# Optimization experiments

Measured on AMD Instinct MI355X. Metric: run time of the kernel, lower is better.

## Reference

```python
import jax, jax.numpy as jnp
import numpy as np
import math

DIM = 768
MAX_STEP = 4
B, S = 32, 2048
LN_EPS = 1e-5
NORM_EPS = 1e-12


def _ln_relu(x, g, b):
    mu = jnp.mean(x, axis=-1, keepdims=True)
    var = jnp.mean((x - mu) ** 2, axis=-1, keepdims=True)
    return jax.nn.relu((x - mu) * jax.lax.rsqrt(var + LN_EPS) * g + b)


def _l2norm(v):  # torch F.normalize along dim=1
    n = jnp.sqrt(jnp.sum(v * v, axis=1, keepdims=True))
    return v / jnp.maximum(n, NORM_EPS)


def setup_inputs() -> dict:
    key = jax.random.key(0)
    ks = jax.random.split(key, 16)
    d = DIM
    inp = {
        "step": 0,
        "context": jax.random.normal(ks[0], (B, S, d), jnp.float32),
        "question": jax.random.normal(ks[1], (B, d), jnp.float32),
        "control": jax.random.normal(ks[2], (B, 2 * d), jnp.float32),
        "qm1": jax.random.randint(ks[3], (B, S), 0, 2).astype(jnp.float32),
        "qm2": jax.random.randint(ks[4], (B, S), 0, 2).astype(jnp.float32),
        "qm_l1": jax.random.randint(ks[5], (B,), 0, S).astype(jnp.int32),
        "qm_l2": jax.random.randint(ks[6], (B,), 0, S).astype(jnp.int32),
        # parameters (xavier-ish scale)
        "W_pos": jax.random.normal(ks[7], (MAX_STEP, d, d), jnp.float32) * (1.0 / math.sqrt(d)),
        "b_pos": jnp.zeros((MAX_STEP, d), jnp.float32),
        "ln1_g": jnp.ones((d,), jnp.float32), "ln1_b": jnp.zeros((d,), jnp.float32),
        "W_cq": jax.random.normal(ks[8], (3 * d, d), jnp.float32) * (1.0 / math.sqrt(3 * d)),
        "b_cq": jnp.zeros((d,), jnp.float32),
        "ln2_g": jnp.ones((d,), jnp.float32), "ln2_b": jnp.zeros((d,), jnp.float32),
        "W_attn": jax.random.normal(ks[9], (d, 1), jnp.float32) * (1.0 / math.sqrt(d)),
        "b_attn": jnp.zeros((1,), jnp.float32),
        "W_fuse": jax.random.normal(ks[10], (2 * d, d), jnp.float32) * (1.0 / math.sqrt(2 * d)),
        "b_fuse": jnp.zeros((d,), jnp.float32),
        "ln3_g": jnp.ones((d,), jnp.float32), "ln3_b": jnp.zeros((d,), jnp.float32),
        "ln4_g": jnp.ones((d,), jnp.float32), "ln4_b": jnp.zeros((d,), jnp.float32),
    }
    return inp


def reference(step, context, question, control, qm1, qm2, qm_l1, qm_l2,
              W_pos, b_pos, ln1_g, ln1_b, W_cq, b_cq, ln2_g, ln2_b,
              W_attn, b_attn, W_fuse, b_fuse, ln3_g, ln3_b, ln4_g, ln4_b):
    d = context.shape[-1]
    scale = 1.0 / math.sqrt(d)
    qm = qm1 + qm2  # [B,S]

    pa = _ln_relu(question @ W_pos[step] + b_pos[step], ln1_g, ln1_b)  # [B,d]
    cq = _ln_relu(jnp.concatenate([control, pa], axis=1) @ W_cq + b_cq, ln2_g, ln2_b)
    cqu = cq[:, None, :]  # [B,1,d]

    def scores(x, mask):  # x:[B,S,d], mask:[B,S]
        w = (x @ W_attn + b_attn) * scale  # [B,S,1] (dropout is identity in eval)
        w = jnp.where(mask[:, :, None] == 0, -1e9, w)
        return jax.nn.softmax(w, axis=1)

    attn = scores(cqu * context, qm)                     # [B,S,1]
    masked_ctx1 = context * qm1[:, :, None]
    masked_ctx2 = context * qm2[:, :, None]
    attn1 = scores(cqu * masked_ctx1, qm1)
    attn2 = scores(cqu * masked_ctx2, qm2)

    mc1 = _l2norm(jnp.sum(attn1 * masked_ctx1, axis=1))  # [B,d]
    mc2 = _l2norm(jnp.sum(attn2 * masked_ctx2, axis=1))
    ncf = _l2norm(jnp.sum(attn * context, axis=1))

    ctrl1 = _ln_relu(jnp.concatenate([mc1, ncf], axis=1) @ W_fuse + b_fuse, ln3_g, ln3_b)
    ctrl2 = _ln_relu(jnp.concatenate([mc2, ncf], axis=1) @ W_fuse + b_fuse, ln4_g, ln4_b)

    next_control = jnp.concatenate([ctrl1, ctrl2], axis=1)  # [B,2d]
    attentions = jnp.concatenate([attn[:, None], attn1[:, None], attn2[:, None]], axis=1)  # [B,3,S,1]
    return next_control, attentions
```

## Files before the change

### kernel.cpp

```cpp
#include <hip/hip_runtime.h>
#include <hip/hip_bf16.h>
#include <math.h>

#define DIM   768
#define BATCH 32
#define SEQ   2048
#define SCALE 0.036084391824351615f

__device__ __forceinline__ float wave_sum(float v) {
#pragma unroll
    for (int o = 32; o > 0; o >>= 1) v += __shfl_xor(v, o, 64);
    return v;
}

__device__ __forceinline__ void fma4(float4& a, float s, const float4& c) {
    a.x += s * c.x; a.y += s * c.y; a.z += s * c.z; a.w += s * c.w;
}

__global__ __launch_bounds__(256) void gemm_partial(
        const float* __restrict__ A0, int lda0,
        const float* __restrict__ A1, int lda1, int ksplit,
        const float* __restrict__ W,
        float* __restrict__ part, int Mtot,
        const int* __restrict__ step_ptr, int wstride) {
    const float* Wp = W + (step_ptr ? (long)step_ptr[0] * wstride : 0);
    const int jt = blockIdx.x * 64;
    const int r0 = blockIdx.y * 32;
    const int kc = blockIdx.z;
    __shared__ float As[32][33];
    __shared__ float Ws[32][64];
    const int t = threadIdx.x;
    const int j = t & 63;
    const int bg = t >> 6;
    float acc[8];
#pragma unroll
    for (int i = 0; i < 8; i++) acc[i] = 0.f;

    for (int k0 = kc * 64; k0 < kc * 64 + 64; k0 += 32) {
        {
            int r  = t >> 3;
            int kk = (t & 7) * 4;
            int ka = k0 + kk;
            float4 av;
            if (ka < ksplit)
                av = *(const float4*)(A0 + (long)(r0 + r) * lda0 + ka);
            else
                av = *(const float4*)(A1 + (long)(r0 + r) * lda1 + (ka - ksplit));
            As[r][kk] = av.x; As[r][kk + 1] = av.y; As[r][kk + 2] = av.z; As[r][kk + 3] = av.w;
        }
#pragma unroll
        for (int i = 0; i < 2; i++) {
            int idx = t + i * 256;
            int row = idx >> 4, col4 = idx & 15;
            float4 wv = *(const float4*)(Wp + (long)(k0 + row) * DIM + jt + col4 * 4);
            *(float4*)&Ws[row][col4 * 4] = wv;
        }
        __syncthreads();
#pragma unroll 8
        for (int kk = 0; kk < 32; kk++) {
            float wv = Ws[kk][j];
#pragma unroll
            for (int i = 0; i < 8; i++) acc[i] += As[bg * 8 + i][kk] * wv;
        }
        __syncthreads();
    }
#pragma unroll
    for (int i = 0; i < 8; i++)
        part[((long)(kc * Mtot + r0 + bg * 8 + i)) * DIM + jt + j] = acc[i];
}

__global__ __launch_bounds__(256) void reduce_ln(
        const float* __restrict__ part, int KC, int Mtot,
        const float* __restrict__ bias,
        const int* __restrict__ step_ptr, int bstride,
        const float* __restrict__ g, const float* __restrict__ b,
        const float* __restrict__ wattn,
        float* __restrict__ out) {
    const int row = blockIdx.x;
    const int t = threadIdx.x;
    const float* bp = bias + (step_ptr ? (long)step_ptr[0] * bstride : 0);
    __shared__ float r1[4], r2[4];
    float x[3];
    float s = 0.f, ss = 0.f;
#pragma unroll
    for (int i = 0; i < 3; i++) {
        int jj = t + i * 256;
        float v = bp[jj];
#pragma unroll 4
        for (int kc = 0; kc < KC; kc++)
            v += part[((long)(kc * Mtot + row)) * DIM + jj];
        x[i] = v; s += v; ss += v * v;
    }
    float wsv = wave_sum(s), wss = wave_sum(ss);
    int lane = t & 63, wid = t >> 6;
    if (lane == 0) { r1[wid] = wsv; r2[wid] = wss; }
    __syncthreads();
    s  = r1[0] + r1[1] + r1[2] + r1[3];
    ss = r2[0] + r2[1] + r2[2] + r2[3];
    float mu = s * (1.f / DIM);
    float var = ss * (1.f / DIM) - mu * mu;
    float rs = rsqrtf(var + 1e-5f);
#pragma unroll
    for (int i = 0; i < 3; i++) {
        int jj = t + i * 256;
        float y = (x[i] - mu) * rs * g[jj] + b[jj];
        y = y > 0.f ? y : 0.f;
        if (wattn) y *= wattn[jj];
        out[(long)row * DIM + jj] = y;
    }
}

__global__ __launch_bounds__(256) void reduce_ln_final(
        const float* __restrict__ part, int KC,
        const float* __restrict__ bias,
        const float* __restrict__ g3, const float* __restrict__ b3,
        const float* __restrict__ g4, const float* __restrict__ b4,
        float* __restrict__ nc) {
    const int row = blockIdx.x;
    const int t = threadIdx.x;
    __shared__ float r1[4], r2[4];
    float x[3];
    float s = 0.f, ss = 0.f;
#pragma unroll
    for (int i = 0; i < 3; i++) {
        int jj = t + i * 256;
        float v = bias[jj];
#pragma unroll 4
        for (int kc = 0; kc < KC; kc++)
            v += part[((long)(kc * 64 + row)) * DIM + jj];
        x[i] = v; s += v; ss += v * v;
    }
    float wsv = wave_sum(s), wss = wave_sum(ss);
    int lane = t & 63, wid = t >> 6;
    if (lane == 0) { r1[wid] = wsv; r2[wid] = wss; }
    __syncthreads();
    s  = r1[0] + r1[1] + r1[2] + r1[3];
    ss = r2[0] + r2[1] + r2[2] + r2[3];
    float mu = s * (1.f / DIM);
    float var = ss * (1.f / DIM) - mu * mu;
    float rs = rsqrtf(var + 1e-5f);
    const float* g  = (row < 32) ? g3 : g4;
    const float* bb = (row < 32) ? b3 : b4;
    int bidx = row & 31;
    int off  = (row < 32) ? 0 : DIM;
#pragma unroll
    for (int i = 0; i < 3; i++) {
        int jj = t + i * 256;
        float y = (x[i] - mu) * rs * g[jj] + bb[jj];
        nc[(long)bidx * (2 * DIM) + off + jj] = y > 0.f ? y : 0.f;
    }
}

__global__ __launch_bounds__(512, 4) void attn_main(
        const float* __restrict__ ctx, const float* __restrict__ part2,
        const float* __restrict__ b_cq,
        const float* __restrict__ ln2_g, const float* __restrict__ ln2_b,
        const float* __restrict__ W_attn, const float* __restrict__ b_attn,
        const float* __restrict__ qm1, const float* __restrict__ qm2,
        float* __restrict__ w, float* __restrict__ zpart,
        float* __restrict__ pvec) {
    const int c = blockIdx.x;
    const int b = blockIdx.y;
    const int t = threadIdx.x;
    const int wave = t >> 6, lane = t & 63;
    __shared__ float4 red[3][192];
    __shared__ float ush[DIM];
    __shared__ float sc1[8], sc2[8];

    {
        float ua = b_cq[t];
        float ub = (t < 256) ? b_cq[t + 512] : 0.f;
#pragma unroll 4
        for (int kc = 0; kc < 36; kc++) {
            const float* p2 = part2 + ((long)(kc * 32 + b)) * DIM;
            ua += p2[t];
            if (t < 256) ub += p2[t + 512];
        }
        float v1 = wave_sum(ua + ub);
        float v2 = wave_sum(ua * ua + ub * ub);
        if (lane == 0) { sc1[wave] = v1; sc2[wave] = v2; }
        __syncthreads();
        float s = 0.f, ss = 0.f;
#pragma unroll
        for (int i = 0; i < 8; i++) { s += sc1[i]; ss += sc2[i]; }
        float mu = s * (1.f / DIM);
        float var = ss * (1.f / DIM) - mu * mu;
        float rs = rsqrtf(var + 1e-5f);
        float y = (ua - mu) * rs * ln2_g[t] + ln2_b[t];
        ush[t] = (y > 0.f ? y : 0.f) * W_attn[t];
        if (t < 256) {
            float y2 = (ub - mu) * rs * ln2_g[t + 512] + ln2_b[t + 512];
            ush[t + 512] = (y2 > 0.f ? y2 : 0.f) * W_attn[t + 512];
        }
        __syncthreads();
    }

    const float batt = b_attn[0];
    const long row0 = (long)b * SEQ + c * 128;

    float4 uu[3];
#pragma unroll
    for (int i = 0; i < 3; i++)
        uu[i] = ((const float4*)ush)[lane + i * 64];

    float4 acc[3][3];
#pragma unroll
    for (int k = 0; k < 3; k++)
#pragma unroll
        for (int i = 0; i < 3; i++) acc[k][i] = make_float4(0.f, 0.f, 0.f, 0.f);
    float zacc[3] = {0.f, 0.f, 0.f};

#pragma unroll 1
    for (int g = 0; g < 4; g++) {
        const int rw = g * 32 + wave * 4;
        float4 cr[4][3];
        float d[4];
#pragma unroll
        for (int rr = 0; rr < 4; rr++) {
            const float4* crow = (const float4*)(ctx + (row0 + rw + rr) * DIM);
            float dd = 0.f;
#pragma unroll
            for (int i = 0; i < 3; i++) {
                float4 cv = crow[lane + i * 64];
                cr[rr][i] = cv;
                dd += cv.x * uu[i].x + cv.y * uu[i].y + cv.z * uu[i].z + cv.w * uu[i].w;
            }
            d[rr] = wave_sum(dd);
        }
        float lw0 = (d[0] + batt) * SCALE;
        float lw1 = (d[1] + batt) * SCALE;
        float lw2 = (d[2] + batt) * SCALE;
        float lw3 = (d[3] + batt) * SCALE;
        if (lane < 4) {
            float v = lane == 0 ? lw0 : lane == 1 ? lw1 : lane == 2 ? lw2 : lw3;
            w[row0 + rw + lane] = v;
        }
        float mv = 0.f;
        if (lane < 4) mv = qm1[row0 + rw + lane];
        else if (lane < 8) mv = qm2[row0 + rw + lane - 4];
#pragma unroll
        for (int rr = 0; rr < 4; rr++) {
            float a1 = __shfl(mv, rr, 64);
            float a2 = __shfl(mv, rr + 4, 64);
            float lwr = rr == 0 ? lw0 : rr == 1 ? lw1 : rr == 2 ? lw2 : lw3;
            float ev = __expf(lwr);
            float e0 = (a1 != 0.f || a2 != 0.f) ? ev : 0.f;
            float e1 = (a1 != 0.f) ? ev : 0.f;
            float e2 = (a2 != 0.f) ? ev : 0.f;
            zacc[0] += e0; zacc[1] += e1; zacc[2] += e2;
#pragma unroll
            for (int i = 0; i < 3; i++) {
                fma4(acc[0][i], e0, cr[rr][i]);
                fma4(acc[1][i], e1, cr[rr][i]);
                fma4(acc[2][i], e2, cr[rr][i]);
            }
        }
    }
    if (lane == 0) {
        float* zp = zpart + ((long)(b * 16 + c) * 8 + wave) * 3;
        zp[0] = zacc[0]; zp[1] = zacc[1]; zp[2] = zacc[2];
    }
    if (wave == 0) {
#pragma unroll
        for (int k = 0; k < 3; k++)
#pragma unroll
            for (int i = 0; i < 3; i++) red[k][lane + i * 64] = acc[k][i];
    }
    __syncthreads();
#pragma unroll 1
    for (int wv = 1; wv < 8; wv++) {
        if (wave == wv) {
#pragma unroll
            for (int k = 0; k < 3; k++)
#pragma unroll
                for (int i = 0; i < 3; i++) {
                    float4 r = red[k][lane + i * 64];
                    r.x += acc[k][i].x; r.y += acc[k][i].y;
                    r.z += acc[k][i].z; r.w += acc[k][i].w;
                    red[k][lane + i * 64] = r;
                }
        }
        __syncthreads();
    }
    for (int idx = t; idx < 576; idx += 512) {
        int k = idx / 192, col = idx - k * 192;
        ((float4*)pvec)[((long)(b * 16 + c) * 3 + k) * 192 + col] = red[k][col];
    }
}

__global__ __launch_bounds__(256) void combine_norm(
        const float* __restrict__ zpart, const float* __restrict__ pvec,
        const float* __restrict__ w,
        const float* __restrict__ qm1, const float* __restrict__ qm2,
        float* __restrict__ A6, float* __restrict__ attn_out) {
    const int b = blockIdx.x, k = blockIdx.y;
    const int t = threadIdx.x;
    const int lane = t & 63, wid = t >> 6;
    __shared__ float r1[4], r2[4];
    float z = 0.f;
    for (int j = t; j < 128; j += 256)
        z += zpart[((long)b * 128 + j) * 3 + k];
    z = wave_sum(z);
    if (lane == 0) r1[wid] = z;
    __syncthreads();
    z = r1[0] + r1[1] + r1[2] + r1[3];
    float v[3] = {0.f, 0.f, 0.f};
    for (int cch = 0; cch < 16; cch++) {
        const float* p = pvec + ((long)(b * 16 + cch) * 3 + k) * DIM;
#pragma unroll
        for (int i = 0; i < 3; i++) v[i] += p[t + i * 256];
    }
    float ss = v[0] * v[0] + v[1] * v[1] + v[2] * v[2];
    float wss = wave_sum(ss);
    if (lane == 0) r2[wid] = wss;
    __syncthreads();
    ss = r2[0] + r2[1] + r2[2] + r2[3];
    float inv = 1.f / fmaxf(sqrtf(ss), 1e-12f);
#pragma unroll
    for (int i = 0; i < 3; i++) {
        int jj = t + i * 256;
        float nv = v[i] * inv;
        if (k == 0) {
            A6[(long)b * (2 * DIM) + DIM + jj] = nv;
            A6[(long)(32 + b) * (2 * DIM) + DIM + jj] = nv;
        } else if (k == 1) {
            A6[(long)b * (2 * DIM) + jj] = nv;
        } else {
            A6[(long)(32 + b) * (2 * DIM) + jj] = nv;
        }
    }
    float iz = 1.f / z;
#pragma unroll
    for (int ii = 0; ii < 8; ii++) {
        int s = t + ii * 256;
        float wv = w[(long)b * SEQ + s];
        float m1 = qm1[(long)b * SEQ + s];
        float m2 = qm2[(long)b * SEQ + s];
        bool act = (k == 0) ? (m1 != 0.f || m2 != 0.f) : (k == 1) ? (m1 != 0.f) : (m2 != 0.f);
        attn_out[((long)b * 3 + k) * SEQ + s] = act ? __expf(wv) * iz : 0.f;
    }
}

extern "C" void kernel_launch(void* const* d_in, const int* in_sizes, int n_in,
                              void* d_out, int out_size, void* d_ws, size_t ws_size,
                              hipStream_t stream) {
    const int*   step     = (const int*)  d_in[0];
    const float* ctx      = (const float*)d_in[1];
    const float* question = (const float*)d_in[2];
    const float* control  = (const float*)d_in[3];
    const float* qm1      = (const float*)d_in[4];
    const float* qm2      = (const float*)d_in[5];
    const float* W_pos    = (const float*)d_in[8];
    const float* b_pos    = (const float*)d_in[9];
    const float* ln1_g    = (const float*)d_in[10];
    const float* ln1_b    = (const float*)d_in[11];
    const float* W_cq     = (const float*)d_in[12];
    const float* b_cq     = (const float*)d_in[13];
    const float* ln2_g    = (const float*)d_in[14];
    const float* ln2_b    = (const float*)d_in[15];
    const float* W_attn   = (const float*)d_in[16];
    const float* b_attn   = (const float*)d_in[17];
    const float* W_fuse   = (const float*)d_in[18];
    const float* b_fuse   = (const float*)d_in[19];
    const float* ln3_g    = (const float*)d_in[20];
    const float* ln3_b    = (const float*)d_in[21];
    const float* ln4_g    = (const float*)d_in[22];
    const float* ln4_b    = (const float*)d_in[23];

    float* ws    = (float*)d_ws;
    float* pa    = ws;
    float* w     = ws + 49152;
    float* zpart = ws + 114688;
    float* A6    = ws + 126976;
    float* part2 = ws + 225280;
    float* big   = ws + 1110016;

    float* nc_out   = (float*)d_out;
    float* attn_out = (float*)d_out + BATCH * 2 * DIM;

    gemm_partial<<<dim3(DIM / 64, 1, DIM / 64), 256, 0, stream>>>(
        question, DIM, question, DIM, 1 << 30, W_pos, big, 32, step, DIM * DIM);
    reduce_ln<<<BATCH, 256, 0, stream>>>(big, DIM / 64, 32, b_pos, step, DIM,
                                         ln1_g, ln1_b, nullptr, pa);

    gemm_partial<<<dim3(DIM / 64, 1, (3 * DIM) / 64), 256, 0, stream>>>(
        control, 2 * DIM, pa, DIM, 2 * DIM, W_cq, part2, 32, nullptr, 0);

    attn_main<<<dim3(SEQ / 128, BATCH), 512, 0, stream>>>(
        ctx, part2, b_cq, ln2_g, ln2_b, W_attn, b_attn, qm1, qm2, w, zpart, big);

    combine_norm<<<dim3(BATCH, 3), 256, 0, stream>>>(
        zpart, big, w, qm1, qm2, A6, attn_out);

    gemm_partial<<<dim3(DIM / 64, 2, (2 * DIM) / 64), 256, 0, stream>>>(
        A6, 2 * DIM, A6, 2 * DIM, 1 << 30, W_fuse, big, 64, nullptr, 0);
    reduce_ln_final<<<2 * BATCH, 256, 0, stream>>>(big, (2 * DIM) / 64, b_fuse,
                                                   ln3_g, ln3_b, ln4_g, ln4_b, nc_out);
}
```

Before: 94.54 us.

## Merge pre-attention GEMMs and fuse LN1 into the W_cq pa-slice GEMM

The W_pos GEMM and the control part of the W_cq GEMM now run in one launch, because neither depends on the other. The W_pos split-K now uses 4 chunks of 192 instead of 12. A new kernel reduces the W_pos partials, applies LayerNorm+ReLU in shared memory and multiplies the pa slice against the last third of W_cq, writing into the same partial buffer. This drops one launch and the pa round trip to global memory. In exchange, each block recomputes the row statistics redundantly, and the longer K-loops in the first launch reduce parallelism.

Result: slower. 108.0 us (+14.3%).

```diff
diff --git a/kernel.cpp b/kernel.cpp
--- a/kernel.cpp
+++ b/kernel.cpp
@@ -17,97 +17,157 @@
     a.x += s * c.x; a.y += s * c.y; a.z += s * c.z; a.w += s * c.w;
 }
 
+__device__ __forceinline__ void gemm_range(
+        float (*As)[33], float (*Ws)[64],
+        const float* __restrict__ A, int lda,
+        const float* __restrict__ W,
+        float* __restrict__ part, int Mtot, int r0, int jt,
+        int kbeg, int kend, int kcidx) {
+    const int t = threadIdx.x;
+    const int j = t & 63;
+    const int bg = t >> 6;
+    float acc[8];
+#pragma unroll
+    for (int i = 0; i < 8; i++) acc[i] = 0.f;
+
+    for (int k0 = kbeg; k0 < kend; k0 += 32) {
+        {
+            int r  = t >> 3;
+            int kk = (t & 7) * 4;
+            float4 av = *(const float4*)(A + (long)(r0 + r) * lda + k0 + kk);
+            As[r][kk] = av.x; As[r][kk + 1] = av.y; As[r][kk + 2] = av.z; As[r][kk + 3] = av.w;
+        }
+#pragma unroll
+        for (int i = 0; i < 2; i++) {
+            int idx = t + i * 256;
+            int row = idx >> 4, col4 = idx & 15;
+            float4 wv = *(const float4*)(W + (long)(k0 + row) * DIM + jt + col4 * 4);
+            *(float4*)&Ws[row][col4 * 4] = wv;
+        }
+        __syncthreads();
+#pragma unroll 8
+        for (int kk = 0; kk < 32; kk++) {
+            float wv = Ws[kk][j];
+#pragma unroll
+            for (int i = 0; i < 8; i++) acc[i] += As[bg * 8 + i][kk] * wv;
+        }
+        __syncthreads();
+    }
+#pragma unroll
+    for (int i = 0; i < 8; i++)
+        part[((long)(kcidx * Mtot + r0 + bg * 8 + i)) * DIM + jt + j] = acc[i];
+}
+
+__global__ __launch_bounds__(256) void k1_kernel(
+        const float* __restrict__ question, const float* __restrict__ W_pos,
+        const int* __restrict__ step_ptr,
+        const float* __restrict__ control, const float* __restrict__ W_cq,
+        float* __restrict__ part1, float* __restrict__ part2) {
+    __shared__ float As[32][33];
+    __shared__ float Ws[32][64];
+    const int i = blockIdx.x;
+    if (i < 48) {
+        const int jt = (i % 12) * 64;
+        const int kc = i / 12;
+        const float* Wp = W_pos + (long)step_ptr[0] * DIM * DIM;
+        gemm_range(As, Ws, question, DIM, Wp, part1, 32, 0, jt,
+                   kc * 192, kc * 192 + 192, kc);
+    } else {
+        const int m = i - 48;
+        const int jt = (m % 12) * 64;
+        const int kc = m / 12;
+        gemm_range(As, Ws, control, 2 * DIM, W_cq, part2, 32, 0, jt,
+                   kc * 64, kc * 64 + 64, kc);
+    }
+}
+
+__global__ __launch_bounds__(256) void gemm2pa_kernel(
+        const float* __restrict__ part1, const float* __restrict__ b_pos,
+        const int* __restrict__ step_ptr,
+        const float* __restrict__ ln1_g, const float* __restrict__ ln1_b,
+        const float* __restrict__ W_cq, float* __restrict__ part2) {
+    const int i = blockIdx.x;
+    const int jt = (i % 12) * 64;
+    const int kcp = i / 12;
+    const int t = threadIdx.x;
+    const int lane = t & 63, wave = t >> 6;
+    const float* bp = b_pos + (long)step_ptr[0] * DIM;
+
+    __shared__ float pa_sh[32][64];
+    __shared__ float Ws[32][64];
+    __shared__ float musha[32], rssha[32];
+
+    for (int r = wave * 8; r < wave * 8 + 8; ++r) {
+        float s = 0.f, ss = 0.f;
+        for (int cb = 0; cb < 12; ++cb) {
+            int col = lane + cb * 64;
+            float v = bp[col];
+#pragma unroll
+            for (int kc = 0; kc < 4; kc++)
+                v += part1[((long)(kc * 32 + r)) * DIM + col];
+            s += v; ss += v * v;
+        }
+        s = wave_sum(s); ss = wave_sum(ss);
+        if (lane == 0) {
+            float mu = s * (1.f / DIM);
+            musha[r] = mu;
+            rssha[r] = rsqrtf(ss * (1.f / DIM) - mu * mu + 1e-5f);
+        }
+    }
+    __syncthreads();
+    {
+        int r  = t >> 3;
+        int c0 = (t & 7) * 8;
+#pragma unroll
+        for (int cc = 0; cc < 8; ++cc) {
+            int col = kcp * 64 + c0 + cc;
+            float v = bp[col];
+#pragma unroll
+            for (int kc = 0; kc < 4; kc++)
+                v += part1[((long)(kc * 32 + r)) * DIM + col];
+            float y = (v - musha[r]) * rssha[r] * ln1_g[col] + ln1_b[col];
+            pa_sh[r][c0 + cc] = y > 0.f ? y : 0.f;
+        }
+    }
+    __syncthreads();
+    const int j = t & 63, bg = t >> 6;
+    float acc[8];
+#pragma unroll
+    for (int q = 0; q < 8; q++) acc[q] = 0.f;
+    const long krow0 = 1536 + (long)kcp * 64;
+    for (int k0 = 0; k0 < 64; k0 += 32) {
+#pragma unroll
+        for (int q = 0; q < 2; q++) {
+            int idx = t + q * 256;
+            int row = idx >> 4, col4 = idx & 15;
+            float4 wv = *(const float4*)(W_cq + (krow0 + k0 + row) * DIM + jt + col4 * 4);
+            *(float4*)&Ws[row][col4 * 4] = wv;
+        }
+        __syncthreads();
+#pragma unroll 8
+        for (int kk = 0; kk < 32; kk++) {
+            float wv = Ws[kk][j];
+#pragma unroll
+            for (int q = 0; q < 8; q++) acc[q] += pa_sh[bg * 8 + q][k0 + kk] * wv;
+        }
+        __syncthreads();
+    }
+#pragma unroll
+    for (int q = 0; q < 8; q++)
+        part2[((long)((24 + kcp) * 32 + bg * 8 + q)) * DIM + jt + j] = acc[q];
+}
+
 __global__ __launch_bounds__(256) void gemm_partial(
         const float* __restrict__ A0, int lda0,
-        const float* __restrict__ A1, int lda1, int ksplit,
         const float* __restrict__ W,
-        float* __restrict__ part, int Mtot,
-        const int* __restrict__ step_ptr, int wstride) {
-    const float* Wp = W + (step_ptr ? (long)step_ptr[0] * wstride : 0);
+        float* __restrict__ part, int Mtot) {
     const int jt = blockIdx.x * 64;
     const int r0 = blockIdx.y * 32;
     const int kc = blockIdx.z;
     __shared__ float As[32][33];
     __shared__ float Ws[32][64];
-    const int t = threadIdx.x;
-    const int j = t & 63;
-    const int bg = t >> 6;
-    float acc[8];
-#pragma unroll
-    for (int i = 0; i < 8; i++) acc[i] = 0.f;
-
-    for (int k0 = kc * 64; k0 < kc * 64 + 64; k0 += 32) {
-        {
-            int r  = t >> 3;
-            int kk = (t & 7) * 4;
-            int ka = k0 + kk;
-            float4 av;
-            if (ka < ksplit)
-                av = *(const float4*)(A0 + (long)(r0 + r) * lda0 + ka);
-            else
-                av = *(const float4*)(A1 + (long)(r0 + r) * lda1 + (ka - ksplit));
-            As[r][kk] = av.x; As[r][kk + 1] = av.y; As[r][kk + 2] = av.z; As[r][kk + 3] = av.w;
-        }
-#pragma unroll
-        for (int i = 0; i < 2; i++) {
-            int idx = t + i * 256;
-            int row = idx >> 4, col4 = idx & 15;
-            float4 wv = *(const float4*)(Wp + (long)(k0 + row) * DIM + jt + col4 * 4);
-            *(float4*)&Ws[row][col4 * 4] = wv;
-        }
-        __syncthreads();
-#pragma unroll 8
-        for (int kk = 0; kk < 32; kk++) {
-            float wv = Ws[kk][j];
-#pragma unroll
-            for (int i = 0; i < 8; i++) acc[i] += As[bg * 8 + i][kk] * wv;
-        }
-        __syncthreads();
-    }
-#pragma unroll
-    for (int i = 0; i < 8; i++)
-        part[((long)(kc * Mtot + r0 + bg * 8 + i)) * DIM + jt + j] = acc[i];
-}
-
-__global__ __launch_bounds__(256) void reduce_ln(
-        const float* __restrict__ part, int KC, int Mtot,
-        const float* __restrict__ bias,
-        const int* __restrict__ step_ptr, int bstride,
-        const float* __restrict__ g, const float* __restrict__ b,
-        const float* __restrict__ wattn,
-        float* __restrict__ out) {
-    const int row = blockIdx.x;
-    const int t = threadIdx.x;
-    const float* bp = bias + (step_ptr ? (long)step_ptr[0] * bstride : 0);
-    __shared__ float r1[4], r2[4];
-    float x[3];
-    float s = 0.f, ss = 0.f;
-#pragma unroll
-    for (int i = 0; i < 3; i++) {
-        int jj = t + i * 256;
-        float v = bp[jj];
-#pragma unroll 4
-        for (int kc = 0; kc < KC; kc++)
-            v += part[((long)(kc * Mtot + row)) * DIM + jj];
-        x[i] = v; s += v; ss += v * v;
-    }
-    float wsv = wave_sum(s), wss = wave_sum(ss);
-    int lane = t & 63, wid = t >> 6;
-    if (lane == 0) { r1[wid] = wsv; r2[wid] = wss; }
-    __syncthreads();
-    s  = r1[0] + r1[1] + r1[2] + r1[3];
-    ss = r2[0] + r2[1] + r2[2] + r2[3];
-    float mu = s * (1.f / DIM);
-    float var = ss * (1.f / DIM) - mu * mu;
-    float rs = rsqrtf(var + 1e-5f);
-#pragma unroll
-    for (int i = 0; i < 3; i++) {
-        int jj = t + i * 256;
-        float y = (x[i] - mu) * rs * g[jj] + b[jj];
-        y = y > 0.f ? y : 0.f;
-        if (wattn) y *= wattn[jj];
-        out[(long)row * DIM + jj] = y;
-    }
+    gemm_range(As, Ws, A0, 2 * DIM, W, part, Mtot, r0, jt,
+               kc * 64, kc * 64 + 64, kc);
 }
 
 __global__ __launch_bounds__(256) void reduce_ln_final(
@@ -368,23 +428,21 @@
     const float* ln4_b    = (const float*)d_in[23];
 
     float* ws    = (float*)d_ws;
-    float* pa    = ws;
-    float* w     = ws + 49152;
-    float* zpart = ws + 114688;
-    float* A6    = ws + 126976;
-    float* part2 = ws + 225280;
-    float* big   = ws + 1110016;
+    float* w     = ws;
+    float* zpart = ws + 65536;
+    float* A6    = ws + 77824;
+    float* part1 = ws + 176128;
+    float* part2 = ws + 274432;
+    float* big   = ws + 1159168;
 
     float* nc_out   = (float*)d_out;
     float* attn_out = (float*)d_out + BATCH * 2 * DIM;
 
-    gemm_partial<<<dim3(DIM / 64, 1, DIM / 64), 256, 0, stream>>>(
-        question, DIM, question, DIM, 1 << 30, W_pos, big, 32, step, DIM * DIM);
-    reduce_ln<<<BATCH, 256, 0, stream>>>(big, DIM / 64, 32, b_pos, step, DIM,
-                                         ln1_g, ln1_b, nullptr, pa);
-
-    gemm_partial<<<dim3(DIM / 64, 1, (3 * DIM) / 64), 256, 0, stream>>>(
-        control, 2 * DIM, pa, DIM, 2 * DIM, W_cq, part2, 32, nullptr, 0);
+    k1_kernel<<<336, 256, 0, stream>>>(
+        question, W_pos, step, control, W_cq, part1, part2);
+
+    gemm2pa_kernel<<<144, 256, 0, stream>>>(
+        part1, b_pos, step, ln1_g, ln1_b, W_cq, part2);
 
     attn_main<<<dim3(SEQ / 128, BATCH), 512, 0, stream>>>(
         ctx, part2, b_cq, ln2_g, ln2_b, W_attn, b_attn, qm1, qm2, w, zpart, big);
@@ -393,7 +451,7 @@
         zpart, big, w, qm1, qm2, A6, attn_out);
 
     gemm_partial<<<dim3(DIM / 64, 2, (2 * DIM) / 64), 256, 0, stream>>>(
-        A6, 2 * DIM, A6, 2 * DIM, 1 << 30, W_fuse, big, 64, nullptr, 0);
+        A6, 2 * DIM, W_fuse, big, 64);
     reduce_ln_final<<<2 * BATCH, 256, 0, stream>>>(big, (2 * DIM) / 64, b_fuse,
                                                    ln3_g, ln3_b, ln4_g, ln4_b, nc_out);
 }
```
